# Performance work log

Measured on AMD Instinct MI355X. Metric: run time of the kernel, lower is better.

Reference implementation:

```python
import jax, jax.numpy as jnp
import numpy as np

H = 32  # hidden_size fixed by the module
I = 1   # input_size

def setup_inputs() -> dict:
    key = jax.random.key(0)
    ks = jax.random.split(key, 8)
    B, T = 8192, 512
    s = 0.1
    return {
        "x": jax.random.normal(ks[0], (B, T, I), dtype=jnp.float32),
        "W_ih": jax.random.normal(ks[1], (4 * H, I), dtype=jnp.float32) * s,
        "W_hh": jax.random.normal(ks[2], (4 * H, H), dtype=jnp.float32) * s,
        "b_ih": jax.random.normal(ks[3], (4 * H,), dtype=jnp.float32) * s,
        "b_hh": jax.random.normal(ks[4], (4 * H,), dtype=jnp.float32) * s,
        "W_lin": jax.random.normal(ks[5], (1, H), dtype=jnp.float32) * s,
        "b_lin": jax.random.normal(ks[6], (1,), dtype=jnp.float32) * s,
    }

def _lstm_last_hidden(x, W_ih, W_hh, b_ih, b_hh):
    B = x.shape[0]
    # Precompute input contribution to all gates: [B, T, 4H] -> scan over T.
    xg = jnp.einsum('bti,gi->btg', x, W_ih) + b_ih + b_hh
    xg = jnp.swapaxes(xg, 0, 1)  # [T, B, 4H]

    def step(carry, xg_t):
        h, c = carry
        gates = xg_t + h @ W_hh.T  # [B, 4H]
        i, f, g, o = jnp.split(gates, 4, axis=-1)  # PyTorch gate order i,f,g,o
        i = jax.nn.sigmoid(i)
        f = jax.nn.sigmoid(f)
        g = jnp.tanh(g)
        o = jax.nn.sigmoid(o)
        c = f * c + i * g
        h = o * jnp.tanh(c)
        return (h, c), None

    h0 = jnp.zeros((B, H), dtype=x.dtype)
    c0 = jnp.zeros((B, H), dtype=x.dtype)
    (h_last, _), _ = jax.lax.scan(step, (h0, c0), xg)
    return h_last  # [B, H] == out[:, -1, :]

def reference(x, W_ih, W_hh, b_ih, b_hh, W_lin, b_lin):
    h_last = _lstm_last_hidden(x, W_ih, W_hh, b_ih, b_hh)
    return h_last @ W_lin.T + b_lin  # [B, 1]
```

## Files before the change

### kernel.cpp

```cpp
#include <hip/hip_runtime.h>


#define L2E 1.4426950408889634f

typedef _Float16 f16x8 __attribute__((ext_vector_type(8)));
typedef float    f32x4 __attribute__((ext_vector_type(4)));

__global__ __launch_bounds__(256, 4) void lstm_ct4r(
    const float* __restrict__ x,
    const float* __restrict__ W_ih,
    const float* __restrict__ W_hh,
    const float* __restrict__ b_ih,
    const float* __restrict__ b_hh,
    const float* __restrict__ W_lin,
    const float* __restrict__ b_lin,
    float* __restrict__ out)
{
    __shared__ float xs[512 * 17];
    __shared__ __align__(16) unsigned int hb[2][16 * 20];
    __shared__ float ps[64];

    const int tid  = threadIdx.x;
    const int wv   = tid >> 6;
    const int lane = tid & 63;
    const int col  = lane & 15;
    const int quad = lane >> 4;
    const int base = blockIdx.x * 16;

    {
        const float4* xg = (const float4*)(x + (size_t)base * 512);
        #pragma unroll
        for (int it = 0; it < 8; ++it) {
            int idx = it * 256 + tid;
            float4 v = xg[idx];
            int b  = idx >> 7;
            int t0 = (idx & 127) * 4;
            xs[(t0 + 0) * 17 + b] = v.x;
            xs[(t0 + 1) * 17 + b] = v.y;
            xs[(t0 + 2) * 17 + b] = v.z;
            xs[(t0 + 3) * 17 + b] = v.w;
        }
    }

    f16x8 wA[2];
    #pragma unroll
    for (int tau = 0; tau < 2; ++tau) {
        const int rt = col & 3;
        const float s = (rt == 2) ? (2.0f * L2E) : L2E;
        const int grow = 32 * rt + 8 * wv + 2 * (col >> 2) + tau;
        #pragma unroll
        for (int j = 0; j < 8; ++j)
            wA[tau][j] = (_Float16)(W_hh[grow * 32 + quad * 8 + j] * s);
    }
    const int j0 = 8 * wv + 2 * quad;
    float wih[2][4], bia[2][4];
    #pragma unroll
    for (int tau = 0; tau < 2; ++tau)
        #pragma unroll
        for (int r = 0; r < 4; ++r) {
            const float s = (r == 2) ? (2.0f * L2E) : L2E;
            const int g = 32 * r + j0 + tau;
            wih[tau][r] = W_ih[g] * s;
            bia[tau][r] = (b_ih[g] + b_hh[g]) * s;
        }
    const float wl0 = W_lin[j0], wl1 = W_lin[j0 + 1];

    __syncthreads();

    float c0 = 0.0f, c1 = 0.0f, h0 = 0.0f, h1 = 0.0f;
    f16x8 bfrag = {};
    f32x4 cq[2];
    {
        float xt = xs[col];
        #pragma unroll
        for (int tau = 0; tau < 2; ++tau)
            #pragma unroll
            for (int r = 0; r < 4; ++r)
                cq[tau][r] = fmaf(xt, wih[tau][r], bia[tau][r]);
    }

    const int wr = col * 20 + 4 * wv + quad;

    #pragma unroll 4
    for (int t = 0; t < 512; ++t) {
        unsigned int* buf = hb[t & 1];

        f32x4 a0 = __builtin_amdgcn_mfma_f32_16x16x32_f16(wA[0], bfrag, cq[0], 0, 0, 0);
        f32x4 a1 = __builtin_amdgcn_mfma_f32_16x16x32_f16(wA[1], bfrag, cq[1], 0, 0, 0);

        float xt1 = xs[((t + 1) & 511) * 17 + col];

        float ei0 = __builtin_amdgcn_exp2f(-a0[0]);
        float ef0 = __builtin_amdgcn_exp2f(-a0[1]);
        float eg0 = __builtin_amdgcn_exp2f(-a0[2]);
        float eo0 = __builtin_amdgcn_exp2f(-a0[3]);
        float ei1 = __builtin_amdgcn_exp2f(-a1[0]);
        float ef1 = __builtin_amdgcn_exp2f(-a1[1]);
        float eg1 = __builtin_amdgcn_exp2f(-a1[2]);
        float eo1 = __builtin_amdgcn_exp2f(-a1[3]);
        float aI0 = 1.0f + ei0, aF0 = 1.0f + ef0, aG0 = 1.0f + eg0, aO0 = 1.0f + eo0;
        float aI1 = 1.0f + ei1, aF1 = 1.0f + ef1, aG1 = 1.0f + eg1, aO1 = 1.0f + eo1;
        float tIG0 = aI0 * aG0, tIG1 = aI1 * aG1;
        float num0 = fmaf(c0, tIG0, (1.0f - eg0) * aF0);
        float num1 = fmaf(c1, tIG1, (1.0f - eg1) * aF1);
        float D0 = aF0 * tIG0, D1 = aF1 * tIG1;
        float rD = __builtin_amdgcn_rcpf(D0 * D1);
        c0 = num0 * (rD * D1);
        c1 = num1 * (rD * D0);
        float ec0 = __builtin_amdgcn_exp2f(c0 * (-2.0f * L2E));
        float ec1 = __builtin_amdgcn_exp2f(c1 * (-2.0f * L2E));
        float H0 = aO0 * (1.0f + ec0), H1 = aO1 * (1.0f + ec1);
        float rH = __builtin_amdgcn_rcpf(H0 * H1);
        h0 = (1.0f - ec0) * (rH * H1);
        h1 = (1.0f - ec1) * (rH * H0);

        buf[wr] = __builtin_bit_cast(unsigned int, __builtin_amdgcn_cvt_pkrtz(h0, h1));

        #pragma unroll
        for (int tau = 0; tau < 2; ++tau)
            #pragma unroll
            for (int r = 0; r < 4; ++r)
                cq[tau][r] = fmaf(xt1, wih[tau][r], bia[tau][r]);

        __syncthreads();
        uint4 bv = *(const uint4*)&buf[col * 20 + quad * 4];
        bfrag = __builtin_bit_cast(f16x8, bv);
    }

    float v = fmaf(h0, wl0, h1 * wl1);
    v += __shfl_xor(v, 16);
    v += __shfl_xor(v, 32);
    if (lane < 16) ps[wv * 16 + col] = v;
    __syncthreads();
    if (tid < 16)
        out[base + tid] = b_lin[0] + ps[tid] + ps[16 + tid] + ps[32 + tid] + ps[48 + tid];
}

extern "C" void kernel_launch(void* const* d_in, const int* in_sizes, int n_in,
                              void* d_out, int out_size, void* d_ws, size_t ws_size,
                              hipStream_t stream) {
    const float* x     = (const float*)d_in[0];
    const float* W_ih  = (const float*)d_in[1];
    const float* W_hh  = (const float*)d_in[2];
    const float* b_ih  = (const float*)d_in[3];
    const float* b_hh  = (const float*)d_in[4];
    const float* W_lin = (const float*)d_in[5];
    const float* b_lin = (const float*)d_in[6];
    float* out = (float*)d_out;

    const int B = in_sizes[0] / 512;
    dim3 grid(B / 16), block(256);
    lstm_ct4r<<<grid, block, 0, stream>>>(x, W_ih, W_hh, b_ih, b_hh, W_lin, b_lin, out);
}
```

Before: 217.9 us.

## Split block into two 2-wave groups each computing four hidden units

Restructures the work split so each 256-thread block handles 32 sequences as two independent 2-wave groups, with each wave running four MFMAs and four hidden units per step instead of two. The input sequence is staged through double-buffered 128-step LDS chunks refilled inside the loop rather than fully preloaded, cutting shared memory use. This trades fewer total waves and fewer barrier participants per sequence for more serial gate math per wave on the recurrence critical path.

```diff
diff --git a/kernel.cpp b/kernel.cpp
--- a/kernel.cpp
+++ b/kernel.cpp
@@ -6,7 +6,7 @@
 typedef _Float16 f16x8 __attribute__((ext_vector_type(8)));
 typedef float    f32x4 __attribute__((ext_vector_type(4)));
 
-__global__ __launch_bounds__(256, 4) void lstm_ct4r(
+__global__ __launch_bounds__(256, 1) void lstm_2w2g(
     const float* __restrict__ x,
     const float* __restrict__ W_ih,
     const float* __restrict__ W_hh,
@@ -16,79 +16,106 @@
     const float* __restrict__ b_lin,
     float* __restrict__ out)
 {
-    __shared__ float xs[512 * 17];
-    __shared__ __align__(16) unsigned int hb[2][16 * 20];
+    __shared__ float xs[2][2][128][16];
+    __shared__ __align__(16) unsigned int hb[2][2][16 * 20];
     __shared__ float ps[64];
 
     const int tid  = threadIdx.x;
     const int wv   = tid >> 6;
+    const int ga   = wv >> 1;
+    const int wvg  = wv & 1;
     const int lane = tid & 63;
     const int col  = lane & 15;
     const int quad = lane >> 4;
-    const int base = blockIdx.x * 16;
+    const int ltid = tid & 127;
+    const int base = blockIdx.x * 32 + ga * 16;
 
     {
-        const float4* xg = (const float4*)(x + (size_t)base * 512);
-        #pragma unroll
-        for (int it = 0; it < 8; ++it) {
-            int idx = it * 256 + tid;
-            float4 v = xg[idx];
-            int b  = idx >> 7;
-            int t0 = (idx & 127) * 4;
-            xs[(t0 + 0) * 17 + b] = v.x;
-            xs[(t0 + 1) * 17 + b] = v.y;
-            xs[(t0 + 2) * 17 + b] = v.z;
-            xs[(t0 + 3) * 17 + b] = v.w;
-        }
-    }
-
-    f16x8 wA[2];
+        const float* gx = x + (size_t)base * 512;
+        #pragma unroll
+        for (int i = 0; i < 4; ++i) {
+            int idx = i * 128 + ltid;
+            int b   = idx >> 5;
+            int tq  = idx & 31;
+            float4 v = ((const float4*)(gx + (size_t)b * 512))[tq];
+            int t0 = tq * 4;
+            xs[ga][0][t0 + 0][b] = v.x;
+            xs[ga][0][t0 + 1][b] = v.y;
+            xs[ga][0][t0 + 2][b] = v.z;
+            xs[ga][0][t0 + 3][b] = v.w;
+        }
+    }
+
+    f16x8 wA[4];
+    {
+        const int rt = col & 3;
+        const int a  = col >> 2;
+        const float s = (rt == 2) ? (2.0f * L2E) : L2E;
+        #pragma unroll
+        for (int m = 0; m < 4; ++m) {
+            const int grow = 32 * rt + 16 * wvg + 4 * a + m;
+            #pragma unroll
+            for (int j = 0; j < 8; ++j)
+                wA[m][j] = (_Float16)(W_hh[grow * 32 + quad * 8 + j] * s);
+        }
+    }
+
+    float wih[4][4], bia[4][4];
     #pragma unroll
-    for (int tau = 0; tau < 2; ++tau) {
-        const int rt = col & 3;
-        const float s = (rt == 2) ? (2.0f * L2E) : L2E;
-        const int grow = 32 * rt + 8 * wv + 2 * (col >> 2) + tau;
-        #pragma unroll
-        for (int j = 0; j < 8; ++j)
-            wA[tau][j] = (_Float16)(W_hh[grow * 32 + quad * 8 + j] * s);
-    }
-    const int j0 = 8 * wv + 2 * quad;
-    float wih[2][4], bia[2][4];
-    #pragma unroll
-    for (int tau = 0; tau < 2; ++tau)
+    for (int m = 0; m < 4; ++m)
         #pragma unroll
         for (int r = 0; r < 4; ++r) {
             const float s = (r == 2) ? (2.0f * L2E) : L2E;
-            const int g = 32 * r + j0 + tau;
-            wih[tau][r] = W_ih[g] * s;
-            bia[tau][r] = (b_ih[g] + b_hh[g]) * s;
-        }
-    const float wl0 = W_lin[j0], wl1 = W_lin[j0 + 1];
+            const int g = 32 * r + 16 * wvg + 4 * quad + m;
+            wih[m][r] = W_ih[g] * s;
+            bia[m][r] = (b_ih[g] + b_hh[g]) * s;
+        }
 
     __syncthreads();
 
-    float c0 = 0.0f, c1 = 0.0f, h0 = 0.0f, h1 = 0.0f;
+    float c0 = 0.f, c1 = 0.f, c2 = 0.f, c3 = 0.f;
+    float hl0 = 0.f, hl1 = 0.f, hl2 = 0.f, hl3 = 0.f;
     f16x8 bfrag = {};
-    f32x4 cq[2];
+    f32x4 cq[4];
     {
-        float xt = xs[col];
-        #pragma unroll
-        for (int tau = 0; tau < 2; ++tau)
+        float xt = xs[ga][0][0][col];
+        #pragma unroll
+        for (int m = 0; m < 4; ++m)
             #pragma unroll
             for (int r = 0; r < 4; ++r)
-                cq[tau][r] = fmaf(xt, wih[tau][r], bia[tau][r]);
-    }
-
-    const int wr = col * 20 + 4 * wv + quad;
-
-    #pragma unroll 4
+                cq[m][r] = fmaf(xt, wih[m][r], bia[m][r]);
+    }
+
+    const int wr = col * 20 + 8 * wvg + 2 * quad;
+
     for (int t = 0; t < 512; ++t) {
-        unsigned int* buf = hb[t & 1];
+        if ((t & 127) == 0 && t < 384) {
+            const int ck = (t >> 7) + 1;
+            const int cb = ck & 1;
+            const float* gx = x + (size_t)base * 512 + ck * 128;
+            #pragma unroll
+            for (int i = 0; i < 4; ++i) {
+                int idx = i * 128 + ltid;
+                int b   = idx >> 5;
+                int tq  = idx & 31;
+                float4 v = ((const float4*)(gx + (size_t)b * 512))[tq];
+                int t0 = tq * 4;
+                xs[ga][cb][t0 + 0][b] = v.x;
+                xs[ga][cb][t0 + 1][b] = v.y;
+                xs[ga][cb][t0 + 2][b] = v.z;
+                xs[ga][cb][t0 + 3][b] = v.w;
+            }
+        }
+
+        unsigned int* buf = hb[ga][t & 1];
 
         f32x4 a0 = __builtin_amdgcn_mfma_f32_16x16x32_f16(wA[0], bfrag, cq[0], 0, 0, 0);
         f32x4 a1 = __builtin_amdgcn_mfma_f32_16x16x32_f16(wA[1], bfrag, cq[1], 0, 0, 0);
-
-        float xt1 = xs[((t + 1) & 511) * 17 + col];
+        f32x4 a2 = __builtin_amdgcn_mfma_f32_16x16x32_f16(wA[2], bfrag, cq[2], 0, 0, 0);
+        f32x4 a3 = __builtin_amdgcn_mfma_f32_16x16x32_f16(wA[3], bfrag, cq[3], 0, 0, 0);
+
+        const int rt1 = t + 1;
+        float xt1 = xs[ga][(rt1 >> 7) & 1][rt1 & 127][col];
 
         float ei0 = __builtin_amdgcn_exp2f(-a0[0]);
         float ef0 = __builtin_amdgcn_exp2f(-a0[1]);
@@ -111,29 +138,62 @@
         float ec1 = __builtin_amdgcn_exp2f(c1 * (-2.0f * L2E));
         float H0 = aO0 * (1.0f + ec0), H1 = aO1 * (1.0f + ec1);
         float rH = __builtin_amdgcn_rcpf(H0 * H1);
-        h0 = (1.0f - ec0) * (rH * H1);
-        h1 = (1.0f - ec1) * (rH * H0);
-
-        buf[wr] = __builtin_bit_cast(unsigned int, __builtin_amdgcn_cvt_pkrtz(h0, h1));
-
-        #pragma unroll
-        for (int tau = 0; tau < 2; ++tau)
+        hl0 = (1.0f - ec0) * (rH * H1);
+        hl1 = (1.0f - ec1) * (rH * H0);
+        unsigned int pkA = __builtin_bit_cast(unsigned int, __builtin_amdgcn_cvt_pkrtz(hl0, hl1));
+
+        float ei2 = __builtin_amdgcn_exp2f(-a2[0]);
+        float ef2 = __builtin_amdgcn_exp2f(-a2[1]);
+        float eg2 = __builtin_amdgcn_exp2f(-a2[2]);
+        float eo2 = __builtin_amdgcn_exp2f(-a2[3]);
+        float ei3 = __builtin_amdgcn_exp2f(-a3[0]);
+        float ef3 = __builtin_amdgcn_exp2f(-a3[1]);
+        float eg3 = __builtin_amdgcn_exp2f(-a3[2]);
+        float eo3 = __builtin_amdgcn_exp2f(-a3[3]);
+        float aI2 = 1.0f + ei2, aF2 = 1.0f + ef2, aG2 = 1.0f + eg2, aO2 = 1.0f + eo2;
+        float aI3 = 1.0f + ei3, aF3 = 1.0f + ef3, aG3 = 1.0f + eg3, aO3 = 1.0f + eo3;
+        float tIG2 = aI2 * aG2, tIG3 = aI3 * aG3;
+        float num2 = fmaf(c2, tIG2, (1.0f - eg2) * aF2);
+        float num3 = fmaf(c3, tIG3, (1.0f - eg3) * aF3);
+        float D2 = aF2 * tIG2, D3 = aF3 * tIG3;
+        float rD2 = __builtin_amdgcn_rcpf(D2 * D3);
+        c2 = num2 * (rD2 * D3);
+        c3 = num3 * (rD2 * D2);
+        float ec2 = __builtin_amdgcn_exp2f(c2 * (-2.0f * L2E));
+        float ec3 = __builtin_amdgcn_exp2f(c3 * (-2.0f * L2E));
+        float H2 = aO2 * (1.0f + ec2), H3 = aO3 * (1.0f + ec3);
+        float rH2 = __builtin_amdgcn_rcpf(H2 * H3);
+        hl2 = (1.0f - ec2) * (rH2 * H3);
+        hl3 = (1.0f - ec3) * (rH2 * H2);
+        unsigned int pkB = __builtin_bit_cast(unsigned int, __builtin_amdgcn_cvt_pkrtz(hl2, hl3));
+
+        uint2 w2; w2.x = pkA; w2.y = pkB;
+        *(uint2*)&buf[wr] = w2;
+
+        #pragma unroll
+        for (int m = 0; m < 4; ++m)
             #pragma unroll
             for (int r = 0; r < 4; ++r)
-                cq[tau][r] = fmaf(xt1, wih[tau][r], bia[tau][r]);
+                cq[m][r] = fmaf(xt1, wih[m][r], bia[m][r]);
 
         __syncthreads();
         uint4 bv = *(const uint4*)&buf[col * 20 + quad * 4];
         bfrag = __builtin_bit_cast(f16x8, bv);
     }
 
-    float v = fmaf(h0, wl0, h1 * wl1);
+    const int j0 = 16 * wvg + 4 * quad;
+    float v = hl0 * W_lin[j0 + 0];
+    v = fmaf(hl1, W_lin[j0 + 1], v);
+    v = fmaf(hl2, W_lin[j0 + 2], v);
+    v = fmaf(hl3, W_lin[j0 + 3], v);
     v += __shfl_xor(v, 16);
     v += __shfl_xor(v, 32);
     if (lane < 16) ps[wv * 16 + col] = v;
     __syncthreads();
-    if (tid < 16)
-        out[base + tid] = b_lin[0] + ps[tid] + ps[16 + tid] + ps[32 + tid] + ps[48 + tid];
+    if (tid < 32) {
+        const int g2 = tid >> 4, cc = tid & 15;
+        out[blockIdx.x * 32 + tid] = b_lin[0] + ps[g2 * 32 + cc] + ps[g2 * 32 + 16 + cc];
+    }
 }
 
 extern "C" void kernel_launch(void* const* d_in, const int* in_sizes, int n_in,
@@ -149,6 +209,6 @@
     float* out = (float*)d_out;
 
     const int B = in_sizes[0] / 512;
-    dim3 grid(B / 16), block(256);
-    lstm_ct4r<<<grid, block, 0, stream>>>(x, W_ih, W_hh, b_ih, b_hh, W_lin, b_lin, out);
+    dim3 grid(B / 32), block(256);
+    lstm_2w2g<<<grid, block, 0, stream>>>(x, W_ih, W_hh, b_ih, b_hh, W_lin, b_lin, out);
 }
```

Result: slower. 286.1 us (+31.3%).

## Run each 16-sequence LSTM block in one wavefront, keeping hidden state in registers

Applied to the files above, without the earlier changes.

The block shrinks from four wavefronts to a single 64-lane wavefront that owns all 32 hidden units of 16 batch columns. Each step issues eight MFMAs, and the new hidden state is packed straight into the B-fragment register, so the per-step LDS write, __syncthreads and LDS read go away. In exchange each wave does four times the MFMA and activation work on a serial dependency chain, and launch_bounds(64,1) lets register use grow. It also relies on the MFMA output layout lining up with the B-fragment layout with no shuffle, which changes occupancy and latency hiding.

```diff
diff --git a/kernel.cpp b/kernel.cpp
--- a/kernel.cpp
+++ b/kernel.cpp
@@ -6,7 +6,35 @@
 typedef _Float16 f16x8 __attribute__((ext_vector_type(8)));
 typedef float    f32x4 __attribute__((ext_vector_type(4)));
 
-__global__ __launch_bounds__(256, 4) void lstm_ct4r(
+#define ACT_PAIR(A0, A1, C0, C1, H0, H1, PK)                                          \
+    {                                                                                 \
+        float ei0 = __builtin_amdgcn_exp2f(-(A0)[0]);                                 \
+        float ef0 = __builtin_amdgcn_exp2f(-(A0)[1]);                                 \
+        float eg0 = __builtin_amdgcn_exp2f(-(A0)[2]);                                 \
+        float eo0 = __builtin_amdgcn_exp2f(-(A0)[3]);                                 \
+        float ei1 = __builtin_amdgcn_exp2f(-(A1)[0]);                                 \
+        float ef1 = __builtin_amdgcn_exp2f(-(A1)[1]);                                 \
+        float eg1 = __builtin_amdgcn_exp2f(-(A1)[2]);                                 \
+        float eo1 = __builtin_amdgcn_exp2f(-(A1)[3]);                                 \
+        float aI0 = 1.0f + ei0, aF0 = 1.0f + ef0, aG0 = 1.0f + eg0, aO0 = 1.0f + eo0; \
+        float aI1 = 1.0f + ei1, aF1 = 1.0f + ef1, aG1 = 1.0f + eg1, aO1 = 1.0f + eo1; \
+        float tIG0 = aI0 * aG0, tIG1 = aI1 * aG1;                                     \
+        float num0 = fmaf((C0), tIG0, (1.0f - eg0) * aF0);                            \
+        float num1 = fmaf((C1), tIG1, (1.0f - eg1) * aF1);                            \
+        float D0 = aF0 * tIG0, D1 = aF1 * tIG1;                                       \
+        float rD = __builtin_amdgcn_rcpf(D0 * D1);                                    \
+        (C0) = num0 * (rD * D1);                                                      \
+        (C1) = num1 * (rD * D0);                                                      \
+        float ec0 = __builtin_amdgcn_exp2f((C0) * (-2.0f * L2E));                     \
+        float ec1 = __builtin_amdgcn_exp2f((C1) * (-2.0f * L2E));                     \
+        float Hh0 = aO0 * (1.0f + ec0), Hh1 = aO1 * (1.0f + ec1);                     \
+        float rH = __builtin_amdgcn_rcpf(Hh0 * Hh1);                                  \
+        (H0) = (1.0f - ec0) * (rH * Hh1);                                             \
+        (H1) = (1.0f - ec1) * (rH * Hh0);                                             \
+        (PK) = __builtin_bit_cast(unsigned int, __builtin_amdgcn_cvt_pkrtz((H0), (H1))); \
+    }
+
+__global__ __launch_bounds__(64, 1) void lstm_ll(
     const float* __restrict__ x,
     const float* __restrict__ W_ih,
     const float* __restrict__ W_hh,
@@ -17,24 +45,21 @@
     float* __restrict__ out)
 {
     __shared__ float xs[512 * 17];
-    __shared__ __align__(16) unsigned int hb[2][16 * 20];
-    __shared__ float ps[64];
 
     const int tid  = threadIdx.x;
-    const int wv   = tid >> 6;
-    const int lane = tid & 63;
-    const int col  = lane & 15;
-    const int quad = lane >> 4;
+    const int col  = tid & 15;
+    const int quad = tid >> 4;
     const int base = blockIdx.x * 16;
 
     {
         const float4* xg = (const float4*)(x + (size_t)base * 512);
-        #pragma unroll
-        for (int it = 0; it < 8; ++it) {
-            int idx = it * 256 + tid;
-            float4 v = xg[idx];
-            int b  = idx >> 7;
-            int t0 = (idx & 127) * 4;
+        #pragma unroll 4
+        for (int i = 0; i < 32; ++i) {
+            int idx = i * 64 + tid;
+            int b   = idx >> 7;
+            int tq  = idx & 127;
+            float4 v = xg[b * 128 + tq];
+            int t0 = tq * 4;
             xs[(t0 + 0) * 17 + b] = v.x;
             xs[(t0 + 1) * 17 + b] = v.y;
             xs[(t0 + 2) * 17 + b] = v.z;
@@ -42,98 +67,83 @@
         }
     }
 
-    f16x8 wA[2];
+    f16x8 wA[8];
+    {
+        const int r = col & 3;
+        const int a = col >> 2;
+        const float s = (r == 2) ? (2.0f * L2E) : L2E;
+        #pragma unroll
+        for (int m = 0; m < 8; ++m) {
+            const int grow = 32 * r + 8 * a + m;
+            #pragma unroll
+            for (int j = 0; j < 8; ++j)
+                wA[m][j] = (_Float16)(W_hh[grow * 32 + quad * 8 + j] * s);
+        }
+    }
+
+    float wih[8][4], bia[8][4];
     #pragma unroll
-    for (int tau = 0; tau < 2; ++tau) {
-        const int rt = col & 3;
-        const float s = (rt == 2) ? (2.0f * L2E) : L2E;
-        const int grow = 32 * rt + 8 * wv + 2 * (col >> 2) + tau;
-        #pragma unroll
-        for (int j = 0; j < 8; ++j)
-            wA[tau][j] = (_Float16)(W_hh[grow * 32 + quad * 8 + j] * s);
-    }
-    const int j0 = 8 * wv + 2 * quad;
-    float wih[2][4], bia[2][4];
-    #pragma unroll
-    for (int tau = 0; tau < 2; ++tau)
+    for (int m = 0; m < 8; ++m)
         #pragma unroll
         for (int r = 0; r < 4; ++r) {
             const float s = (r == 2) ? (2.0f * L2E) : L2E;
-            const int g = 32 * r + j0 + tau;
-            wih[tau][r] = W_ih[g] * s;
-            bia[tau][r] = (b_ih[g] + b_hh[g]) * s;
+            const int g = 32 * r + 8 * quad + m;
+            wih[m][r] = W_ih[g] * s;
+            bia[m][r] = (b_ih[g] + b_hh[g]) * s;
         }
-    const float wl0 = W_lin[j0], wl1 = W_lin[j0 + 1];
 
     __syncthreads();
 
-    float c0 = 0.0f, c1 = 0.0f, h0 = 0.0f, h1 = 0.0f;
+    float cc[8] = {0.f, 0.f, 0.f, 0.f, 0.f, 0.f, 0.f, 0.f};
+    float hl[8];
     f16x8 bfrag = {};
-    f32x4 cq[2];
+    f32x4 cq[8];
     {
         float xt = xs[col];
         #pragma unroll
-        for (int tau = 0; tau < 2; ++tau)
+        for (int m = 0; m < 8; ++m)
             #pragma unroll
             for (int r = 0; r < 4; ++r)
-                cq[tau][r] = fmaf(xt, wih[tau][r], bia[tau][r]);
+                cq[m][r] = fmaf(xt, wih[m][r], bia[m][r]);
     }
 
-    const int wr = col * 20 + 4 * wv + quad;
-
-    #pragma unroll 4
     for (int t = 0; t < 512; ++t) {
-        unsigned int* buf = hb[t & 1];
-
         f32x4 a0 = __builtin_amdgcn_mfma_f32_16x16x32_f16(wA[0], bfrag, cq[0], 0, 0, 0);
         f32x4 a1 = __builtin_amdgcn_mfma_f32_16x16x32_f16(wA[1], bfrag, cq[1], 0, 0, 0);
+        f32x4 a2 = __builtin_amdgcn_mfma_f32_16x16x32_f16(wA[2], bfrag, cq[2], 0, 0, 0);
+        f32x4 a3 = __builtin_amdgcn_mfma_f32_16x16x32_f16(wA[3], bfrag, cq[3], 0, 0, 0);
+        f32x4 a4 = __builtin_amdgcn_mfma_f32_16x16x32_f16(wA[4], bfrag, cq[4], 0, 0, 0);
+        f32x4 a5 = __builtin_amdgcn_mfma_f32_16x16x32_f16(wA[5], bfrag, cq[5], 0, 0, 0);
+        f32x4 a6 = __builtin_amdgcn_mfma_f32_16x16x32_f16(wA[6], bfrag, cq[6], 0, 0, 0);
+        f32x4 a7 = __builtin_amdgcn_mfma_f32_16x16x32_f16(wA[7], bfrag, cq[7], 0, 0, 0);
 
         float xt1 = xs[((t + 1) & 511) * 17 + col];
 
-        float ei0 = __builtin_amdgcn_exp2f(-a0[0]);
-        float ef0 = __builtin_amdgcn_exp2f(-a0[1]);
-        float eg0 = __builtin_amdgcn_exp2f(-a0[2]);
-        float eo0 = __builtin_amdgcn_exp2f(-a0[3]);
-        float ei1 = __builtin_amdgcn_exp2f(-a1[0]);
-        float ef1 = __builtin_amdgcn_exp2f(-a1[1]);
-        float eg1 = __builtin_amdgcn_exp2f(-a1[2]);
-        float eo1 = __builtin_amdgcn_exp2f(-a1[3]);
-        float aI0 = 1.0f + ei0, aF0 = 1.0f + ef0, aG0 = 1.0f + eg0, aO0 = 1.0f + eo0;
-        float aI1 = 1.0f + ei1, aF1 = 1.0f + ef1, aG1 = 1.0f + eg1, aO1 = 1.0f + eo1;
-        float tIG0 = aI0 * aG0, tIG1 = aI1 * aG1;
-        float num0 = fmaf(c0, tIG0, (1.0f - eg0) * aF0);
-        float num1 = fmaf(c1, tIG1, (1.0f - eg1) * aF1);
-        float D0 = aF0 * tIG0, D1 = aF1 * tIG1;
-        float rD = __builtin_amdgcn_rcpf(D0 * D1);
-        c0 = num0 * (rD * D1);
-        c1 = num1 * (rD * D0);
-        float ec0 = __builtin_amdgcn_exp2f(c0 * (-2.0f * L2E));
-        float ec1 = __builtin_amdgcn_exp2f(c1 * (-2.0f * L2E));
-        float H0 = aO0 * (1.0f + ec0), H1 = aO1 * (1.0f + ec1);
-        float rH = __builtin_amdgcn_rcpf(H0 * H1);
-        h0 = (1.0f - ec0) * (rH * H1);
-        h1 = (1.0f - ec1) * (rH * H0);
+        unsigned int pk0, pk1, pk2, pk3;
+        ACT_PAIR(a0, a1, cc[0], cc[1], hl[0], hl[1], pk0);
+        ACT_PAIR(a2, a3, cc[2], cc[3], hl[2], hl[3], pk1);
+        ACT_PAIR(a4, a5, cc[4], cc[5], hl[4], hl[5], pk2);
+        ACT_PAIR(a6, a7, cc[6], cc[7], hl[6], hl[7], pk3);
 
-        buf[wr] = __builtin_bit_cast(unsigned int, __builtin_amdgcn_cvt_pkrtz(h0, h1));
+        union { f16x8 v; unsigned int u[4]; } bb;
+        bb.u[0] = pk0; bb.u[1] = pk1; bb.u[2] = pk2; bb.u[3] = pk3;
+        bfrag = bb.v;
 
         #pragma unroll
-        for (int tau = 0; tau < 2; ++tau)
+        for (int m = 0; m < 8; ++m)
             #pragma unroll
             for (int r = 0; r < 4; ++r)
-                cq[tau][r] = fmaf(xt1, wih[tau][r], bia[tau][r]);
-
-        __syncthreads();
-        uint4 bv = *(const uint4*)&buf[col * 20 + quad * 4];
-        bfrag = __builtin_bit_cast(f16x8, bv);
+                cq[m][r] = fmaf(xt1, wih[m][r], bia[m][r]);
     }
 
-    float v = fmaf(h0, wl0, h1 * wl1);
+    float v = 0.0f;
+    #pragma unroll
+    for (int j = 0; j < 8; ++j)
+        v = fmaf(hl[j], W_lin[8 * quad + j], v);
     v += __shfl_xor(v, 16);
     v += __shfl_xor(v, 32);
-    if (lane < 16) ps[wv * 16 + col] = v;
-    __syncthreads();
     if (tid < 16)
-        out[base + tid] = b_lin[0] + ps[tid] + ps[16 + tid] + ps[32 + tid] + ps[48 + tid];
+        out[base + col] = v + b_lin[0];
 }
 
 extern "C" void kernel_launch(void* const* d_in, const int* in_sizes, int n_in,
@@ -149,6 +159,6 @@
     float* out = (float*)d_out;
 
     const int B = in_sizes[0] / 512;
-    dim3 grid(B / 16), block(256);
-    lstm_ct4r<<<grid, block, 0, stream>>>(x, W_ih, W_hh, b_ih, b_hh, W_lin, b_lin, out);
+    dim3 grid(B / 16), block(64);
+    lstm_ll<<<grid, block, 0, stream>>>(x, W_ih, W_hh, b_ih, b_hh, W_lin, b_lin, out);
 }
```

Result: slower. 361.8 us (+66.0%).

## Halve batch rows per block to 8 with two-wave blocks and quad MFMAs

Applied to the files above, without the earlier changes.

Each block now processes 8 batch rows with 128 threads (two waves) instead of 16 rows with 256 threads. Each wave issues four MFMAs per step, and the upper half of the lanes selects the second pair of results. The MFMA B columns 8-15 duplicate columns 0-7. The aim is to shrink the per-step barrier to two waves and launch more, smaller blocks, which shortens the recurrence's critical path. In exchange, each wave does twice the MFMA work, much of it redundant, and adds select instructions.

```diff
diff --git a/kernel.cpp b/kernel.cpp
--- a/kernel.cpp
+++ b/kernel.cpp
@@ -6,7 +6,7 @@
 typedef _Float16 f16x8 __attribute__((ext_vector_type(8)));
 typedef float    f32x4 __attribute__((ext_vector_type(4)));
 
-__global__ __launch_bounds__(256, 4) void lstm_ct4r(
+__global__ __launch_bounds__(128, 2) void lstm_g8(
     const float* __restrict__ x,
     const float* __restrict__ W_ih,
     const float* __restrict__ W_hh,
@@ -16,52 +16,57 @@
     const float* __restrict__ b_lin,
     float* __restrict__ out)
 {
-    __shared__ float xs[512 * 17];
-    __shared__ __align__(16) unsigned int hb[2][16 * 20];
-    __shared__ float ps[64];
+    __shared__ float xs[512 * 9];
+    __shared__ __align__(16) unsigned int hb[2][8 * 20];
+    __shared__ float ps[16];
 
     const int tid  = threadIdx.x;
     const int wv   = tid >> 6;
     const int lane = tid & 63;
     const int col  = lane & 15;
+    const int b    = col & 7;
+    const int hi   = col >> 3;
     const int quad = lane >> 4;
-    const int base = blockIdx.x * 16;
+    const int base = blockIdx.x * 8;
 
     {
-        const float4* xg = (const float4*)(x + (size_t)base * 512);
+        const float* gx = x + (size_t)base * 512;
         #pragma unroll
-        for (int it = 0; it < 8; ++it) {
-            int idx = it * 256 + tid;
-            float4 v = xg[idx];
-            int b  = idx >> 7;
-            int t0 = (idx & 127) * 4;
-            xs[(t0 + 0) * 17 + b] = v.x;
-            xs[(t0 + 1) * 17 + b] = v.y;
-            xs[(t0 + 2) * 17 + b] = v.z;
-            xs[(t0 + 3) * 17 + b] = v.w;
+        for (int i = 0; i < 8; ++i) {
+            int bb = i;
+            float4 v = ((const float4*)(gx + (size_t)bb * 512))[tid];
+            int t0 = tid * 4;
+            xs[(t0 + 0) * 9 + bb] = v.x;
+            xs[(t0 + 1) * 9 + bb] = v.y;
+            xs[(t0 + 2) * 9 + bb] = v.z;
+            xs[(t0 + 3) * 9 + bb] = v.w;
         }
     }
 
-    f16x8 wA[2];
-    #pragma unroll
-    for (int tau = 0; tau < 2; ++tau) {
-        const int rt = col & 3;
-        const float s = (rt == 2) ? (2.0f * L2E) : L2E;
-        const int grow = 32 * rt + 8 * wv + 2 * (col >> 2) + tau;
+    f16x8 wA[4];
+    {
+        const int r = col & 3;
+        const int a = col >> 2;
+        const float s = (r == 2) ? (2.0f * L2E) : L2E;
         #pragma unroll
-        for (int j = 0; j < 8; ++j)
-            wA[tau][j] = (_Float16)(W_hh[grow * 32 + quad * 8 + j] * s);
+        for (int n = 0; n < 4; ++n) {
+            const int grow = 32 * r + 16 * wv + 4 * a + n;
+            #pragma unroll
+            for (int j = 0; j < 8; ++j)
+                wA[n][j] = (_Float16)(W_hh[grow * 32 + 8 * quad + j] * s);
+        }
     }
-    const int j0 = 8 * wv + 2 * quad;
+
+    const int j0 = 16 * wv + 4 * quad + 2 * hi;
     float wih[2][4], bia[2][4];
     #pragma unroll
-    for (int tau = 0; tau < 2; ++tau)
+    for (int p = 0; p < 2; ++p)
         #pragma unroll
         for (int r = 0; r < 4; ++r) {
             const float s = (r == 2) ? (2.0f * L2E) : L2E;
-            const int g = 32 * r + j0 + tau;
-            wih[tau][r] = W_ih[g] * s;
-            bia[tau][r] = (b_ih[g] + b_hh[g]) * s;
+            const int g = 32 * r + j0 + p;
+            wih[p][r] = W_ih[g] * s;
+            bia[p][r] = (b_ih[g] + b_hh[g]) * s;
         }
     const float wl0 = W_lin[j0], wl1 = W_lin[j0 + 1];
 
@@ -71,15 +76,16 @@
     f16x8 bfrag = {};
     f32x4 cq[2];
     {
-        float xt = xs[col];
+        float xt = xs[b];
         #pragma unroll
-        for (int tau = 0; tau < 2; ++tau)
+        for (int p = 0; p < 2; ++p)
             #pragma unroll
             for (int r = 0; r < 4; ++r)
-                cq[tau][r] = fmaf(xt, wih[tau][r], bia[tau][r]);
+                cq[p][r] = fmaf(xt, wih[p][r], bia[p][r]);
     }
 
-    const int wr = col * 20 + 4 * wv + quad;
+    const int wr = b * 20 + 8 * wv + 2 * quad + hi;
+    const int rd = b * 20 + 4 * quad;
 
     #pragma unroll 4
     for (int t = 0; t < 512; ++t) {
@@ -87,17 +93,26 @@
 
         f32x4 a0 = __builtin_amdgcn_mfma_f32_16x16x32_f16(wA[0], bfrag, cq[0], 0, 0, 0);
         f32x4 a1 = __builtin_amdgcn_mfma_f32_16x16x32_f16(wA[1], bfrag, cq[1], 0, 0, 0);
+        f32x4 a2 = __builtin_amdgcn_mfma_f32_16x16x32_f16(wA[2], bfrag, cq[0], 0, 0, 0);
+        f32x4 a3 = __builtin_amdgcn_mfma_f32_16x16x32_f16(wA[3], bfrag, cq[1], 0, 0, 0);
 
-        float xt1 = xs[((t + 1) & 511) * 17 + col];
+        float xt1 = xs[((t + 1) & 511) * 9 + b];
 
-        float ei0 = __builtin_amdgcn_exp2f(-a0[0]);
-        float ef0 = __builtin_amdgcn_exp2f(-a0[1]);
-        float eg0 = __builtin_amdgcn_exp2f(-a0[2]);
-        float eo0 = __builtin_amdgcn_exp2f(-a0[3]);
-        float ei1 = __builtin_amdgcn_exp2f(-a1[0]);
-        float ef1 = __builtin_amdgcn_exp2f(-a1[1]);
-        float eg1 = __builtin_amdgcn_exp2f(-a1[2]);
-        float eo1 = __builtin_amdgcn_exp2f(-a1[3]);
+        f32x4 s0, s1;
+        #pragma unroll
+        for (int r = 0; r < 4; ++r) {
+            s0[r] = hi ? a2[r] : a0[r];
+            s1[r] = hi ? a3[r] : a1[r];
+        }
+
+        float ei0 = __builtin_amdgcn_exp2f(-s0[0]);
+        float ef0 = __builtin_amdgcn_exp2f(-s0[1]);
+        float eg0 = __builtin_amdgcn_exp2f(-s0[2]);
+        float eo0 = __builtin_amdgcn_exp2f(-s0[3]);
+        float ei1 = __builtin_amdgcn_exp2f(-s1[0]);
+        float ef1 = __builtin_amdgcn_exp2f(-s1[1]);
+        float eg1 = __builtin_amdgcn_exp2f(-s1[2]);
+        float eo1 = __builtin_amdgcn_exp2f(-s1[3]);
         float aI0 = 1.0f + ei0, aF0 = 1.0f + ef0, aG0 = 1.0f + eg0, aO0 = 1.0f + eo0;
         float aI1 = 1.0f + ei1, aF1 = 1.0f + ef1, aG1 = 1.0f + eg1, aO1 = 1.0f + eo1;
         float tIG0 = aI0 * aG0, tIG1 = aI1 * aG1;
@@ -117,23 +132,24 @@
         buf[wr] = __builtin_bit_cast(unsigned int, __builtin_amdgcn_cvt_pkrtz(h0, h1));
 
         #pragma unroll
-        for (int tau = 0; tau < 2; ++tau)
+        for (int p = 0; p < 2; ++p)
             #pragma unroll
             for (int r = 0; r < 4; ++r)
-                cq[tau][r] = fmaf(xt1, wih[tau][r], bia[tau][r]);
+                cq[p][r] = fmaf(xt1, wih[p][r], bia[p][r]);
 
         __syncthreads();
-        uint4 bv = *(const uint4*)&buf[col * 20 + quad * 4];
+        uint4 bv = *(const uint4*)&buf[rd];
         bfrag = __builtin_bit_cast(f16x8, bv);
     }
 
     float v = fmaf(h0, wl0, h1 * wl1);
+    v += __shfl_xor(v, 8);
     v += __shfl_xor(v, 16);
     v += __shfl_xor(v, 32);
-    if (lane < 16) ps[wv * 16 + col] = v;
+    if (lane < 8) ps[wv * 8 + lane] = v;
     __syncthreads();
-    if (tid < 16)
-        out[base + tid] = b_lin[0] + ps[tid] + ps[16 + tid] + ps[32 + tid] + ps[48 + tid];
+    if (tid < 8)
+        out[base + tid] = b_lin[0] + ps[tid] + ps[8 + tid];
 }
 
 extern "C" void kernel_launch(void* const* d_in, const int* in_sizes, int n_in,
@@ -149,6 +165,6 @@
     float* out = (float*)d_out;
 
     const int B = in_sizes[0] / 512;
-    dim3 grid(B / 16), block(256);
-    lstm_ct4r<<<grid, block, 0, stream>>>(x, W_ih, W_hh, b_ih, b_hh, W_lin, b_lin, out);
+    dim3 grid(B / 8), block(128);
+    lstm_g8<<<grid, block, 0, stream>>>(x, W_ih, W_hh, b_ih, b_hh, W_lin, b_lin, out);
 }
```

After: 259.6 us. 19.1% more time.
